# Optimization experiments

Measured on AMD Instinct MI355X. Metric: run time of the kernel, lower is better.

Reference implementation:

```python
import jax, jax.numpy as jnp
import numpy as np
from jax import lax

NMS_RADIUS = 3
NMS_ITERS = 2


def _maxpool(x, r):
    # nn.MaxPool2d(kernel=2r+1, stride=1, pad=r); torch pads with -inf for max
    k = 2 * r + 1
    return lax.reduce_window(x, -jnp.inf, lax.max,
                             (1, 1, k, k), (1, 1, 1, 1),
                             [(0, 0), (0, 0), (r, r), (r, r)])


def simple_nms(scores, nms_radius=NMS_RADIUS, iteration=NMS_ITERS):
    zeros = jnp.zeros_like(scores)
    max_mask = scores == _maxpool(scores, nms_radius)
    for _ in range(iteration):
        supp_mask = _maxpool(max_mask.astype(scores.dtype), nms_radius) > 0
        supp_scores = jnp.where(supp_mask, zeros, scores)
        new_max_mask = supp_scores == _maxpool(supp_scores, nms_radius)
        max_mask = max_mask | (new_max_mask & ~supp_mask)
    return jnp.where(max_mask, scores, zeros)


def setup_inputs() -> dict:
    key = jax.random.key(0)
    k1, k2, k3 = jax.random.split(key, 3)
    b, h, w, c_feat = 4, 512, 512, 128
    bev = jax.random.normal(k1, (b, 7, h, w), dtype=jnp.float32)
    score_bev_raw = jax.random.uniform(k2, (b, 1, h, w), dtype=jnp.float32)
    feature_bev = jax.random.normal(k3, (b, c_feat, h, w), dtype=jnp.float32)
    return {"bev": bev, "score_bev_raw": score_bev_raw,
            "feature_bev": feature_bev, "num_kpt": 512}


def reference(bev, score_bev_raw, feature_bev, num_kpt):
    b, _, h, w = bev.shape
    guider = (bev[:, 2:3] > 0).astype(bev.dtype)             # [b,1,h,w]
    # points = bev[:,3:7] with z=0, homog=1
    points = jnp.concatenate([bev[:, 3:5],
                              jnp.zeros_like(bev[:, 5:6]),
                              jnp.ones_like(bev[:, 6:7])], axis=1)  # [b,4,h,w]
    score_bev = score_bev_raw * guider                        # [b,1,h,w]
    score_max = simple_nms(score_bev, nms_radius=3)           # [b,1,h,w]
    score2d = score_bev[:, 0]                                 # [b,h,w]
    max2d = score_max[:, 0]
    # valid local maxima: (score == nms_score) & (score > 0)
    mask = (score2d == max2d) & (score2d > 0)
    # vectorized equivalent of per-image where + topk (assumes >= num_kpt valid)
    masked = jnp.where(mask, score2d, -jnp.ones_like(score2d)).reshape(b, h * w)
    _, idx = lax.top_k(masked, num_kpt)                       # [b,k]
    u = idx // w
    v = idx % w
    pixels_kpt = jnp.stack([u, v], axis=-1)                   # [b,k,2]
    pts_flat = points.reshape(b, 4, h * w)
    kpts = jnp.take_along_axis(pts_flat, idx[:, None, :], axis=2)  # [b,4,k]
    kpts = kpts.transpose(0, 2, 1)                            # [b,k,4]
    feat_flat = feature_bev.reshape(b, feature_bev.shape[1], h * w)
    feas_kpt = jnp.take_along_axis(feat_flat, idx[:, None, :], axis=2)  # [b,C,k]
    return score2d, kpts, feas_kpt, pixels_kpt
```

## Files before the change

### kernel.cpp

```cpp
#include <hip/hip_runtime.h>
#include <cfloat>

#define W 512
#define H 512
#define B 4
#define HW (W*H)
#define NTOT (B*HW)
#define CFEAT 128
#define K 512
#define NBINS 65536
#define CAP 49152
#define CNT_STRIDE 16

__global__ void zero_ws_k(unsigned* __restrict__ hist, int* __restrict__ count) {
    int i = blockIdx.x * blockDim.x + threadIdx.x;
    if (i < B * NBINS) hist[i] = 0u;
    if (i < B) count[i * CNT_STRIDE] = 0;
}

__global__ __launch_bounds__(256) void nms_fused_k(
    const float* __restrict__ bev, const float* __restrict__ raw,
    float* __restrict__ out_scores, float* __restrict__ mask_g,
    float* __restrict__ cval, int* __restrict__ cidx,
    int* __restrict__ count, unsigned* __restrict__ hist) {
    __shared__ float SS[62 * 62];
    __shared__ float ST[62 * 62];
    __shared__ float SM[56 * 56];
    __shared__ float SP[50 * 50];
    __shared__ int lcount, lbase;

    const int b = blockIdx.z;
    const int gx0 = blockIdx.x * 32 - 15;
    const int gy0 = blockIdx.y * 32 - 15;
    const int t = threadIdx.x;
    const float* raw_b = raw + b * HW;
    const float* gdr_b = bev + (b * 7 + 2) * HW;

    for (int idx = t; idx < 62 * 62; idx += 256) {
        int y = idx / 62, x = idx - y * 62;
        int gx = gx0 + x, gy = gy0 + y;
        float v = 0.f;
        if ((unsigned)gx < (unsigned)W && (unsigned)gy < (unsigned)H) {
            int g = (gy << 9) + gx;
            v = gdr_b[g] > 0.f ? raw_b[g] : 0.f;
        }
        SS[idx] = v;
    }
    __syncthreads();

#define HMAX7(PTR, STRIDE) ({ const float* _r = (PTR); \
    float _m = fmaxf(fmaxf(fmaxf(_r[-3*(STRIDE)], _r[-2*(STRIDE)]), fmaxf(_r[-(STRIDE)], _r[0])), \
                     fmaxf(fmaxf(_r[(STRIDE)], _r[2*(STRIDE)]), _r[3*(STRIDE)])); _m; })

    for (int idx = t; idx < 62 * 56; idx += 256) {
        int y = idx / 56, x = 3 + (idx - (idx / 56) * 56);
        ST[y * 62 + x] = HMAX7(SS + y * 62 + x, 1);
    }
    __syncthreads();
    for (int idx = t; idx < 56 * 56; idx += 256) {
        int y = 3 + idx / 56, x = 3 + (idx % 56);
        float m = HMAX7(ST + y * 62 + x, 62);
        int gx = gx0 + x, gy = gy0 + y;
        bool inb = (unsigned)gx < (unsigned)W && (unsigned)gy < (unsigned)H;
        SM[(y - 3) * 56 + (x - 3)] = (inb && SS[y * 62 + x] == m) ? 1.f : 0.f;
    }
    __syncthreads();

    for (int idx = t; idx < 56 * 50; idx += 256) {
        int y = 3 + idx / 50, x = 6 + (idx % 50);
        ST[y * 62 + x] = HMAX7(SM + (y - 3) * 56 + (x - 3), 1);
    }
    __syncthreads();
    for (int idx = t; idx < 50 * 50; idx += 256) {
        int y = 6 + idx / 50, x = 6 + (idx % 50);
        float m = HMAX7(ST + y * 62 + x, 62);
        SP[(y - 6) * 50 + (x - 6)] = m > 0.f ? 1.f : 0.f;
    }
    __syncthreads();

    for (int idx = t; idx < 50 * 44; idx += 256) {
        int y = 6 + idx / 44, x = 9 + (idx % 44);
        float m = -FLT_MAX;
#pragma unroll
        for (int dx = -3; dx <= 3; ++dx) {
            int xx = x + dx;
            float s = SP[(y - 6) * 50 + (xx - 6)] > 0.f ? 0.f : SS[y * 62 + xx];
            m = fmaxf(m, s);
        }
        ST[y * 62 + x] = m;
    }
    __syncthreads();
    for (int idx = t; idx < 44 * 44; idx += 256) {
        int y = 9 + idx / 44, x = 9 + (idx % 44);
        float m = HMAX7(ST + y * 62 + x, 62);
        float sup = SP[(y - 6) * 50 + (x - 6)];
        float ss = sup > 0.f ? 0.f : SS[y * 62 + x];
        bool nm = (ss == m) && (sup == 0.f);
        int gx = gx0 + x, gy = gy0 + y;
        bool inb = (unsigned)gx < (unsigned)W && (unsigned)gy < (unsigned)H;
        int mi = (y - 3) * 56 + (x - 3);
        SM[mi] = (SM[mi] > 0.f || (nm && inb)) ? 1.f : 0.f;
    }
    __syncthreads();

    for (int idx = t; idx < 44 * 38; idx += 256) {
        int y = 9 + idx / 38, x = 12 + (idx % 38);
        ST[y * 62 + x] = HMAX7(SM + (y - 3) * 56 + (x - 3), 1);
    }
    __syncthreads();
    for (int idx = t; idx < 38 * 38; idx += 256) {
        int y = 12 + idx / 38, x = 12 + (idx % 38);
        float m = HMAX7(ST + y * 62 + x, 62);
        SP[(y - 12) * 38 + (x - 12)] = m > 0.f ? 1.f : 0.f;
    }
    __syncthreads();

    for (int idx = t; idx < 38 * 32; idx += 256) {
        int y = 12 + idx / 32, x = 15 + (idx % 32);
        float m = -FLT_MAX;
#pragma unroll
        for (int dx = -3; dx <= 3; ++dx) {
            int xx = x + dx;
            float s = SP[(y - 12) * 38 + (xx - 12)] > 0.f ? 0.f : SS[y * 62 + xx];
            m = fmaxf(m, s);
        }
        ST[y * 62 + x] = m;
    }
    __syncthreads();

    float vloc[4]; int gloc[4]; int nloc = 0;
#pragma unroll
    for (int q = 0; q < 4; ++q) {
        int idx = t + q * 256;
        int y = 15 + idx / 32, x = 15 + (idx % 32);
        float m = HMAX7(ST + y * 62 + x, 62);
        float sup = SP[(y - 12) * 38 + (x - 12)];
        float v = SS[y * 62 + x];
        float ss = sup > 0.f ? 0.f : v;
        bool nm = (ss == m) && (sup == 0.f);
        bool mk = (SM[(y - 3) * 56 + (x - 3)] > 0.f) || nm;
        int gx = gx0 + x, gy = gy0 + y;
        int g = (gy << 9) + gx;
        out_scores[b * HW + g] = v;
        mask_g[b * HW + g] = mk ? 1.f : 0.f;
        if (mk && v > 0.f) { vloc[nloc] = v; gloc[nloc] = g; ++nloc; }
    }
    if (t == 0) lcount = 0;
    __syncthreads();
    int p0 = nloc ? atomicAdd(&lcount, nloc) : 0;
    __syncthreads();
    if (t == 0) lbase = lcount ? atomicAdd(&count[b * CNT_STRIDE], lcount) : 0;
    __syncthreads();
    for (int j = 0; j < nloc; ++j) {
        int p = lbase + p0 + j;
        float v = vloc[j];
        if (p < CAP) { cval[b * CAP + p] = v; cidx[b * CAP + p] = gloc[j]; }
        unsigned bin = (unsigned)(v * 65536.f);
        if (bin > 65535u) bin = 65535u;
        atomicAdd(&hist[b * NBINS + bin], 1u);
    }
#undef HMAX7
}

__global__ __launch_bounds__(512) void select_k(
    const float* __restrict__ cval, const int* __restrict__ cidx,
    const int* __restrict__ count, const unsigned* __restrict__ hist,
    const float* __restrict__ scores, const float* __restrict__ mask,
    const float* __restrict__ bev,
    float* __restrict__ out_kpts, float* __restrict__ out_pix, int* __restrict__ topk_idx) {
    __shared__ float sval[1024];
    __shared__ int   sidx[1024];
    __shared__ unsigned part[512];
    __shared__ int final_idx[K];
    __shared__ int nsel_s, tbin_s;

    int b = blockIdx.x, t = threadIdx.x;
    int total = count[b * CNT_STRIDE];
    if (total > CAP) total = CAP;
    const unsigned* Hh = hist + b * NBINS;

    unsigned s = 0;
    const int SPAN = NBINS / 512;
#pragma unroll 4
    for (int i = 0; i < SPAN; ++i) s += Hh[t * SPAN + i];
    part[t] = s;
    if (t == 0) nsel_s = 0;
    __syncthreads();

    if (t == 0) {
        if (total <= K) {
            tbin_s = 0;
        } else {
            unsigned acc = 0; int seg = 0; unsigned before = 0;
            for (int sg = 511; sg >= 0; --sg) {
                if (acc + part[sg] >= (unsigned)K) { seg = sg; before = acc; break; }
                acc += part[sg];
            }
            int base = seg * SPAN;
            unsigned a2 = before; int T = base;
            for (int bin = base + SPAN - 1; bin >= base; --bin) {
                a2 += Hh[bin];
                if (a2 >= (unsigned)K) { T = bin; break; }
            }
            tbin_s = T;
        }
    }
    __syncthreads();
    int tb = tbin_s;

    for (int i = t; i < total; i += 512) {
        float v = cval[b * CAP + i];
        unsigned bin = (unsigned)(v * 65536.f);
        if (bin > 65535u) bin = 65535u;
        if ((int)bin >= tb) {
            int p = atomicAdd(&nsel_s, 1);
            if (p < 1024) { sval[p] = v; sidx[p] = cidx[b * CAP + i]; }
        }
    }
    __syncthreads();
    int ns = nsel_s < 1024 ? nsel_s : 1024;
    for (int i = t; i < 1024; i += 512)
        if (i >= ns) { sval[i] = -FLT_MAX; sidx[i] = 0x40000000 + i; }
    __syncthreads();

    for (int kk = 2; kk <= 1024; kk <<= 1) {
        for (int j = kk >> 1; j > 0; j >>= 1) {
            for (int idx = t; idx < 1024; idx += 512) {
                int p = idx ^ j;
                if (p > idx) {
                    float va = sval[idx], vb = sval[p];
                    int ia = sidx[idx], ib = sidx[p];
                    bool up = ((idx & kk) == 0);
                    bool b_first = (vb > va) || (vb == va && ib < ia);
                    if (b_first == up) {
                        sval[idx] = vb; sval[p] = va;
                        sidx[idx] = ib; sidx[p] = ia;
                    }
                }
            }
            __syncthreads();
        }
    }

    int valid = total < K ? total : K;
    if (t < valid) final_idx[t] = sidx[t];
    __syncthreads();
    if (t == 0 && valid < K) {
        int fill = valid;
        for (int flat = 0; fill < K && flat < HW; ++flat) {
            int gi = b * HW + flat;
            bool cand = (mask[gi] > 0.f) && (scores[gi] > 0.f);
            if (!cand) final_idx[fill++] = flat;
        }
    }
    __syncthreads();

    int flat = final_idx[t];
    int u = flat >> 9, v = flat & (W - 1);
    float p0 = bev[((b * 7 + 3) << 18) + flat];
    float p1 = bev[((b * 7 + 4) << 18) + flat];
    int kb = b * K + t;
    out_kpts[kb * 4 + 0] = p0;
    out_kpts[kb * 4 + 1] = p1;
    out_kpts[kb * 4 + 2] = 0.f;
    out_kpts[kb * 4 + 3] = 1.f;
    out_pix[kb * 2 + 0] = (float)u;
    out_pix[kb * 2 + 1] = (float)v;
    topk_idx[kb] = flat;
}

__global__ __launch_bounds__(512) void gather_k(const float* __restrict__ feat,
                                                const int* __restrict__ topk_idx,
                                                float* __restrict__ out) {
    int c = blockIdx.x, b = blockIdx.y, k = threadIdx.x;
    int flat = topk_idx[b * K + k];
    out[(b * CFEAT + c) * K + k] = feat[((b * CFEAT + c) << 18) + flat];
}

extern "C" void kernel_launch(void* const* d_in, const int* in_sizes, int n_in,
                              void* d_out, int out_size, void* d_ws, size_t ws_size,
                              hipStream_t stream) {
    const float* bev  = (const float*)d_in[0];
    const float* raw  = (const float*)d_in[1];
    const float* feat = (const float*)d_in[2];

    float* out = (float*)d_out;
    float* out_scores = out;
    float* out_kpts   = out + NTOT;
    float* out_feas   = out + NTOT + B * K * 4;
    float* out_pix    = out + NTOT + B * K * 4 + B * CFEAT * K;

    char* w = (char*)d_ws;
    float*    mask  = (float*)(w);
    unsigned* hist  = (unsigned*)(w + 4u * 1024 * 1024);
    int*      count = (int*)(w + 5u * 1024 * 1024);
    float*    cval  = (float*)(w + 5u * 1024 * 1024 + 256);
    int*      cidx  = (int*)(w + 5u * 1024 * 1024 + 256 + B * CAP * 4);
    int*      topk  = (int*)(w + 5u * 1024 * 1024 + 256 + 2u * B * CAP * 4);

    zero_ws_k<<<(B * NBINS + 255) / 256, 256, 0, stream>>>(hist, count);
    nms_fused_k<<<dim3(W / 32, H / 32, B), 256, 0, stream>>>(
        bev, raw, out_scores, mask, cval, cidx, count, hist);
    select_k<<<B, 512, 0, stream>>>(cval, cidx, count, hist, out_scores, mask, bev,
                                    out_kpts, out_pix, topk);
    gather_k<<<dim3(CFEAT, B), 512, 0, stream>>>(feat, topk, out_feas);
}
```

Before: 693.9 us.

## Shrink histogram, pack NMS mask into ballot bits, replace bitonic sort with rank select

The score histogram shrinks from 65536 to 512 bins, so zeroing it and finding the threshold become a small parallel suffix scan instead of serial scans. The float mask written per pixel becomes a wave ballot bitmask, which cuts global writes. The bitonic sort is replaced by a packed 64-bit key with counting-rank selection over up to 2048 candidates. Coarser bins can admit more candidates past the threshold, and the rank step costs O(n^2) in shared memory.

```diff
diff --git a/kernel.cpp b/kernel.cpp
--- a/kernel.cpp
+++ b/kernel.cpp
@@ -8,9 +8,10 @@
 #define NTOT (B*HW)
 #define CFEAT 128
 #define K 512
-#define NBINS 65536
+#define NBINS 512
 #define CAP 49152
 #define CNT_STRIDE 16
+#define NSEL_CAP 2048
 
 __global__ void zero_ws_k(unsigned* __restrict__ hist, int* __restrict__ count) {
     int i = blockIdx.x * blockDim.x + threadIdx.x;
@@ -20,7 +21,7 @@
 
 __global__ __launch_bounds__(256) void nms_fused_k(
     const float* __restrict__ bev, const float* __restrict__ raw,
-    float* __restrict__ out_scores, float* __restrict__ mask_g,
+    float* __restrict__ out_scores, unsigned* __restrict__ maskbits,
     float* __restrict__ cval, int* __restrict__ cidx,
     int* __restrict__ count, unsigned* __restrict__ hist) {
     __shared__ float SS[62 * 62];
@@ -132,7 +133,7 @@
 #pragma unroll
     for (int q = 0; q < 4; ++q) {
         int idx = t + q * 256;
-        int y = 15 + idx / 32, x = 15 + (idx % 32);
+        int y = 15 + (idx >> 5), x = 15 + (idx & 31);
         float m = HMAX7(ST + y * 62 + x, 62);
         float sup = SP[(y - 12) * 38 + (x - 12)];
         float v = SS[y * 62 + x];
@@ -142,7 +143,9 @@
         int gx = gx0 + x, gy = gy0 + y;
         int g = (gy << 9) + gx;
         out_scores[b * HW + g] = v;
-        mask_g[b * HW + g] = mk ? 1.f : 0.f;
+        unsigned long long bal = __ballot(mk);
+        if ((t & 31) == 0)
+            maskbits[(b << 13) + (gy << 4) + blockIdx.x] = (unsigned)(bal >> (t & 32));
         if (mk && v > 0.f) { vloc[nloc] = v; gloc[nloc] = g; ++nloc; }
     }
     if (t == 0) lcount = 0;
@@ -155,8 +158,8 @@
         int p = lbase + p0 + j;
         float v = vloc[j];
         if (p < CAP) { cval[b * CAP + p] = v; cidx[b * CAP + p] = gloc[j]; }
-        unsigned bin = (unsigned)(v * 65536.f);
-        if (bin > 65535u) bin = 65535u;
+        unsigned bin = (unsigned)(v * (float)NBINS);
+        if (bin > (unsigned)(NBINS - 1)) bin = NBINS - 1;
         atomicAdd(&hist[b * NBINS + bin], 1u);
     }
 #undef HMAX7
@@ -165,91 +168,65 @@
 __global__ __launch_bounds__(512) void select_k(
     const float* __restrict__ cval, const int* __restrict__ cidx,
     const int* __restrict__ count, const unsigned* __restrict__ hist,
-    const float* __restrict__ scores, const float* __restrict__ mask,
+    const float* __restrict__ scores, const unsigned* __restrict__ maskbits,
     const float* __restrict__ bev,
     float* __restrict__ out_kpts, float* __restrict__ out_pix, int* __restrict__ topk_idx) {
-    __shared__ float sval[1024];
-    __shared__ int   sidx[1024];
-    __shared__ unsigned part[512];
+    __shared__ unsigned long long skey[NSEL_CAP];
+    __shared__ unsigned suf[NBINS];
     __shared__ int final_idx[K];
     __shared__ int nsel_s, tbin_s;
 
     int b = blockIdx.x, t = threadIdx.x;
     int total = count[b * CNT_STRIDE];
     if (total > CAP) total = CAP;
-    const unsigned* Hh = hist + b * NBINS;
-
-    unsigned s = 0;
-    const int SPAN = NBINS / 512;
-#pragma unroll 4
-    for (int i = 0; i < SPAN; ++i) s += Hh[t * SPAN + i];
-    part[t] = s;
-    if (t == 0) nsel_s = 0;
-    __syncthreads();
-
-    if (t == 0) {
-        if (total <= K) {
-            tbin_s = 0;
-        } else {
-            unsigned acc = 0; int seg = 0; unsigned before = 0;
-            for (int sg = 511; sg >= 0; --sg) {
-                if (acc + part[sg] >= (unsigned)K) { seg = sg; before = acc; break; }
-                acc += part[sg];
-            }
-            int base = seg * SPAN;
-            unsigned a2 = before; int T = base;
-            for (int bin = base + SPAN - 1; bin >= base; --bin) {
-                a2 += Hh[bin];
-                if (a2 >= (unsigned)K) { T = bin; break; }
-            }
-            tbin_s = T;
-        }
+
+    suf[t] = hist[(b << 9) + t];
+    if (t == 0) { nsel_s = 0; tbin_s = 0; }
+    __syncthreads();
+
+    for (int off = 1; off < NBINS; off <<= 1) {
+        unsigned add = (t + off < NBINS) ? suf[t + off] : 0u;
+        __syncthreads();
+        suf[t] += add;
+        __syncthreads();
+    }
+    if (total > K) {
+        unsigned s0 = suf[t];
+        unsigned s1 = (t < NBINS - 1) ? suf[t + 1] : 0u;
+        if (s0 >= (unsigned)K && (t == NBINS - 1 || s1 < (unsigned)K)) tbin_s = t;
     }
     __syncthreads();
     int tb = tbin_s;
 
     for (int i = t; i < total; i += 512) {
         float v = cval[b * CAP + i];
-        unsigned bin = (unsigned)(v * 65536.f);
-        if (bin > 65535u) bin = 65535u;
-        if ((int)bin >= tb) {
+        int bin = (int)(v * (float)NBINS); if (bin > NBINS - 1) bin = NBINS - 1;
+        if (bin >= tb) {
             int p = atomicAdd(&nsel_s, 1);
-            if (p < 1024) { sval[p] = v; sidx[p] = cidx[b * CAP + i]; }
-        }
-    }
-    __syncthreads();
-    int ns = nsel_s < 1024 ? nsel_s : 1024;
-    for (int i = t; i < 1024; i += 512)
-        if (i >= ns) { sval[i] = -FLT_MAX; sidx[i] = 0x40000000 + i; }
-    __syncthreads();
-
-    for (int kk = 2; kk <= 1024; kk <<= 1) {
-        for (int j = kk >> 1; j > 0; j >>= 1) {
-            for (int idx = t; idx < 1024; idx += 512) {
-                int p = idx ^ j;
-                if (p > idx) {
-                    float va = sval[idx], vb = sval[p];
-                    int ia = sidx[idx], ib = sidx[p];
-                    bool up = ((idx & kk) == 0);
-                    bool b_first = (vb > va) || (vb == va && ib < ia);
-                    if (b_first == up) {
-                        sval[idx] = vb; sval[p] = va;
-                        sidx[idx] = ib; sidx[p] = ia;
-                    }
-                }
-            }
-            __syncthreads();
-        }
-    }
-
+            if (p < NSEL_CAP)
+                skey[p] = ((unsigned long long)__float_as_uint(v) << 32)
+                        | (unsigned)(~cidx[b * CAP + i]);
+        }
+    }
+    __syncthreads();
+    int ns = nsel_s < NSEL_CAP ? nsel_s : NSEL_CAP;
     int valid = total < K ? total : K;
-    if (t < valid) final_idx[t] = sidx[t];
-    __syncthreads();
+
+    for (int i = t; i < ns; i += 512) {
+        unsigned long long ki = skey[i];
+        int rank = 0;
+        for (int j = 0; j < ns; ++j)
+            rank += (skey[j] > ki) ? 1 : 0;
+        if (rank < valid) final_idx[rank] = (int)(~(unsigned)ki);
+    }
+    __syncthreads();
+
     if (t == 0 && valid < K) {
         int fill = valid;
         for (int flat = 0; fill < K && flat < HW; ++flat) {
-            int gi = b * HW + flat;
-            bool cand = (mask[gi] > 0.f) && (scores[gi] > 0.f);
+            int gy = flat >> 9, gx = flat & (W - 1);
+            unsigned wb = maskbits[(b << 13) + (gy << 4) + (gx >> 5)];
+            bool cand = ((wb >> (gx & 31)) & 1u) && (scores[b * HW + flat] > 0.f);
             if (!cand) final_idx[fill++] = flat;
         }
     }
@@ -291,17 +268,17 @@
     float* out_pix    = out + NTOT + B * K * 4 + B * CFEAT * K;
 
     char* w = (char*)d_ws;
-    float*    mask  = (float*)(w);
-    unsigned* hist  = (unsigned*)(w + 4u * 1024 * 1024);
-    int*      count = (int*)(w + 5u * 1024 * 1024);
-    float*    cval  = (float*)(w + 5u * 1024 * 1024 + 256);
-    int*      cidx  = (int*)(w + 5u * 1024 * 1024 + 256 + B * CAP * 4);
-    int*      topk  = (int*)(w + 5u * 1024 * 1024 + 256 + 2u * B * CAP * 4);
+    unsigned* maskbits = (unsigned*)(w);
+    unsigned* hist     = (unsigned*)(w + (128u << 10));
+    int*      count    = (int*)(w + (136u << 10));
+    float*    cval     = (float*)(w + (136u << 10) + 256);
+    int*      cidx     = (int*)(w + (136u << 10) + 256 + B * CAP * 4);
+    int*      topk     = (int*)(w + (136u << 10) + 256 + 2u * B * CAP * 4);
 
     zero_ws_k<<<(B * NBINS + 255) / 256, 256, 0, stream>>>(hist, count);
     nms_fused_k<<<dim3(W / 32, H / 32, B), 256, 0, stream>>>(
-        bev, raw, out_scores, mask, cval, cidx, count, hist);
-    select_k<<<B, 512, 0, stream>>>(cval, cidx, count, hist, out_scores, mask, bev,
+        bev, raw, out_scores, maskbits, cval, cidx, count, hist);
+    select_k<<<B, 512, 0, stream>>>(cval, cidx, count, hist, out_scores, maskbits, bev,
                                     out_kpts, out_pix, topk);
     gather_k<<<dim3(CFEAT, B), 512, 0, stream>>>(feat, topk, out_feas);
 }
```

After: 703.6 us. About the same (+1.4%).
